# Performance work log

Hardware: AMD Instinct MI355X
Metric: run time of the kernel (lower is better)

Reference implementation:

```python
import jax, jax.numpy as jnp
import numpy as np

B, EMBED, HIDDEN, C, E = 1024, 768, 2048, 200, 256
LS = 0.1  # rbf_lengthscale
EPS = 1e-5


def setup_inputs() -> dict:
    key = jax.random.key(0)
    ks = jax.random.split(key, 10)
    inp = {
        'features': jax.random.normal(ks[0], (B, EMBED), jnp.float32),
        # MLP layer 1: LayerNorm(EMBED) -> Linear(EMBED, HIDDEN)
        'ln1_g': jnp.ones((EMBED,), jnp.float32),
        'ln1_b': jnp.zeros((EMBED,), jnp.float32),
        'W1': jax.random.normal(ks[1], (EMBED, HIDDEN), jnp.float32) / np.sqrt(EMBED),
        'b1': jnp.zeros((HIDDEN,), jnp.float32),
        # MLP layer 2: LayerNorm(HIDDEN) -> Linear(HIDDEN, HIDDEN)
        'ln2_g': jnp.ones((HIDDEN,), jnp.float32),
        'ln2_b': jnp.zeros((HIDDEN,), jnp.float32),
        'W2': jax.random.normal(ks[2], (HIDDEN, HIDDEN), jnp.float32) / np.sqrt(HIDDEN),
        'b2': jnp.zeros((HIDDEN,), jnp.float32),
        # final projection to centroid_dim
        'W3': jax.random.normal(ks[3], (HIDDEN, E), jnp.float32) / np.sqrt(HIDDEN),
        'b3': jnp.zeros((E,), jnp.float32),
        # per-class transform + centroids (as in torch init)
        'class_weight': jax.random.normal(ks[4], (C, E, E), jnp.float32) * 0.01,
        'centroids': jax.random.normal(ks[5], (C, E), jnp.float32) * 0.05,
    }
    return inp


def _layernorm(x, g, b):
    mu = jnp.mean(x, axis=-1, keepdims=True)
    var = jnp.var(x, axis=-1, keepdims=True)
    return (x - mu) * jax.lax.rsqrt(var + EPS) * g + b


def reference(features, ln1_g, ln1_b, W1, b1, ln2_g, ln2_b, W2, b2, W3, b3,
              class_weight, centroids):
    # feature_extractor MLP (dropout is identity at inference)
    h = _layernorm(features, ln1_g, ln1_b)
    h = jax.nn.gelu(h @ W1 + b1, approximate=False)
    h = _layernorm(h, ln2_g, ln2_b)
    h = jax.nn.gelu(h @ W2 + b2, approximate=False)
    z = h @ W3 + b3  # [B, E]

    # per-class transform: einsum('bce,ced->bcd') with z broadcast over C
    weighted = jnp.einsum('be,ced->bcd', z, class_weight)  # [B, C, E]
    diff = weighted - centroids[None, :, :]
    dist_sq = jnp.sum(diff * diff, axis=-1)  # [B, C]
    log_kernel = -dist_sq / (2.0 * LS * LS)
    kernel_vals = jnp.exp(log_kernel)
    probs = jax.nn.softmax(log_kernel, axis=-1)
    uncertainty = 1.0 - jnp.max(kernel_vals, axis=-1)
    return probs, probs[None], kernel_vals, uncertainty
```

## Files before the change

kernel.cpp:

```cpp
#include <hip/hip_runtime.h>
#include <math.h>

#define B_      1024
#define EMBED_  768
#define HIDDEN_ 2048
#define C_      200
#define E_      256
#define EPS_    1e-5f
#define NEG_INV_2LS2 (-50.0f)

typedef unsigned short ushort_t;
typedef __attribute__((ext_vector_type(8))) short short8;
typedef __attribute__((ext_vector_type(4))) float f32x4;

__device__ __forceinline__ float gelu_exact(float x) {
    return 0.5f * x * (1.0f + erff(x * 0.70710678118654752f));
}

__device__ __forceinline__ ushort_t f2bf(float x) {
    union { float f; unsigned int u; } v; v.f = x;
    unsigned int r = v.u + 0x7fffu + ((v.u >> 16) & 1u);
    return (ushort_t)(r >> 16);
}
__device__ __forceinline__ float bf2f(ushort_t s) {
    union { float f; unsigned int u; } v; v.u = ((unsigned int)s) << 16;
    return v.f;
}

__device__ __forceinline__ void glds16(const void* g, void* l) {
    __builtin_amdgcn_global_load_lds(
        (const __attribute__((address_space(1))) unsigned int*)g,
        (__attribute__((address_space(3))) unsigned int*)l, 16, 0, 0);
}

template<int COLS>
__global__ __launch_bounds__(256)
void ln_split_kernel(const float* __restrict__ x, const float* __restrict__ g,
                     const float* __restrict__ b, ushort_t* __restrict__ oh,
                     ushort_t* __restrict__ ol) {
    const int row = blockIdx.x;
    const int tid = threadIdx.x;
    constexpr int NT  = 256;
    constexpr int PER = COLS / NT;
    float v[PER];
    float s = 0.f, s2 = 0.f;
    const float* xr = x + (size_t)row * COLS;
    #pragma unroll
    for (int i = 0; i < PER; ++i) {
        v[i] = xr[tid + i * NT];
        s  += v[i];
        s2 += v[i] * v[i];
    }
    #pragma unroll
    for (int off = 32; off > 0; off >>= 1) {
        s  += __shfl_down(s,  off, 64);
        s2 += __shfl_down(s2, off, 64);
    }
    __shared__ float sbuf[4], s2buf[4], stat[2];
    const int wid = tid >> 6;
    if ((tid & 63) == 0) { sbuf[wid] = s; s2buf[wid] = s2; }
    __syncthreads();
    if (tid == 0) {
        float ts = 0.f, ts2 = 0.f;
        #pragma unroll
        for (int i = 0; i < NT / 64; ++i) { ts += sbuf[i]; ts2 += s2buf[i]; }
        float mu  = ts / COLS;
        float var = ts2 / COLS - mu * mu;
        stat[0] = mu;
        stat[1] = rsqrtf(var + EPS_);
    }
    __syncthreads();
    const float mu = stat[0], rstd = stat[1];
    #pragma unroll
    for (int i = 0; i < PER; ++i) {
        int c = tid + i * NT;
        float y = (v[i] - mu) * rstd * g[c] + b[c];
        ushort_t h = f2bf(y);
        size_t o = (size_t)row * COLS + c;
        oh[o] = h;
        ol[o] = f2bf(y - bf2f(h));
    }
}

__global__ __launch_bounds__(256)
void tconv_kernel(const float* __restrict__ src, ushort_t* __restrict__ th,
                  ushort_t* __restrict__ tl, int R, int Nc) {
    __shared__ float tile[64][65];
    const size_t base = (size_t)blockIdx.x * R * Nc;
    const int ntx = Nc >> 6;
    const int ky = blockIdx.y / ntx, nx = blockIdx.y % ntx;
    const int tid = threadIdx.x;
    const int col = tid & 63, rr = tid >> 6;
    const float* s = src + base + (size_t)(ky * 64) * Nc + nx * 64;
    #pragma unroll
    for (int i = 0; i < 16; ++i) {
        int r = i * 4 + rr;
        tile[r][col] = s[(size_t)r * Nc + col];
    }
    __syncthreads();
    #pragma unroll
    for (int i = 0; i < 16; ++i) {
        int dl = i * 4 + rr;
        float x = tile[col][dl];
        ushort_t h = f2bf(x);
        size_t o = base + (size_t)(nx * 64 + dl) * R + ky * 64 + col;
        th[o] = h;
        tl[o] = f2bf(x - bf2f(h));
    }
}

template<int MREP, int ACT, int OUT_SPLIT>
__global__ __launch_bounds__(256)
void mfma_gemm_kernel(const ushort_t* __restrict__ Ah, const ushort_t* __restrict__ Al,
                      const ushort_t* __restrict__ Wh, const ushort_t* __restrict__ Wl,
                      const float* __restrict__ bias,
                      float* __restrict__ outF, ushort_t* __restrict__ Oh,
                      ushort_t* __restrict__ Ol, int M, int N, int K) {
    constexpr int BM = MREP * 32;
    __shared__ short AsH[BM * 64], AsL[BM * 64];
    __shared__ short BsH[64 * 64], BsL[64 * 64];
    const int tid  = threadIdx.x;
    const int lane = tid & 63;
    const int w    = tid >> 6;
    const int wr = w >> 1, wc = w & 1;
    const int fr = lane & 15, fg = lane >> 4;

    const int nblk = gridDim.x, chunk = nblk >> 3;
    const int wg = (blockIdx.x & 7) * chunk + (blockIdx.x >> 3);
    const int gy = M / BM;
    const int cx = wg / gy, ry = wg % gy;
    const int row0 = ry * BM, col0 = cx * 64;

    const int srow  = tid >> 3;
    const int sslot = (tid & 7) ^ (srow & 7);
    const size_t aoff = (size_t)(row0 + srow) * K + sslot * 8;
    const size_t boff = (size_t)(col0 + srow) * K + sslot * 8;

    f32x4 acc[MREP][2];
    #pragma unroll
    for (int m = 0; m < MREP; ++m)
        #pragma unroll
        for (int n = 0; n < 2; ++n) acc[m][n] = (f32x4){0.f, 0.f, 0.f, 0.f};

    for (int k0 = 0; k0 < K; k0 += 64) {
        #pragma unroll
        for (int p = 0; p < BM / 32; ++p) {
            glds16(Ah + aoff + (size_t)p * 32 * K + k0, &AsH[p * 2048 + w * 512]);
            glds16(Al + aoff + (size_t)p * 32 * K + k0, &AsL[p * 2048 + w * 512]);
        }
        #pragma unroll
        for (int p = 0; p < 2; ++p) {
            glds16(Wh + boff + (size_t)p * 32 * K + k0, &BsH[p * 2048 + w * 512]);
            glds16(Wl + boff + (size_t)p * 32 * K + k0, &BsL[p * 2048 + w * 512]);
        }
        __syncthreads();
        #pragma unroll
        for (int ks = 0; ks < 2; ++ks) {
            short8 bh[2], bl[2];
            #pragma unroll
            for (int n = 0; n < 2; ++n) {
                int rB = wc * 32 + n * 16 + fr;
                int sl = ((ks * 4 + fg) ^ (rB & 7)) << 3;
                bh[n] = *(const short8*)&BsH[rB * 64 + sl];
                bl[n] = *(const short8*)&BsL[rB * 64 + sl];
            }
            #pragma unroll
            for (int m = 0; m < MREP; ++m) {
                int rA = wr * MREP * 16 + m * 16 + fr;
                int sl = ((ks * 4 + fg) ^ (rA & 7)) << 3;
                short8 ah = *(const short8*)&AsH[rA * 64 + sl];
                short8 al = *(const short8*)&AsL[rA * 64 + sl];
                #pragma unroll
                for (int n = 0; n < 2; ++n) {
                    acc[m][n] = __builtin_amdgcn_mfma_f32_16x16x32_bf16(ah, bh[n], acc[m][n], 0, 0, 0);
                    acc[m][n] = __builtin_amdgcn_mfma_f32_16x16x32_bf16(ah, bl[n], acc[m][n], 0, 0, 0);
                    acc[m][n] = __builtin_amdgcn_mfma_f32_16x16x32_bf16(al, bh[n], acc[m][n], 0, 0, 0);
                }
            }
        }
        __syncthreads();
    }

    #pragma unroll
    for (int n = 0; n < 2; ++n) {
        int col = col0 + wc * 32 + n * 16 + fr;
        float bv = bias[col];
        #pragma unroll
        for (int m = 0; m < MREP; ++m) {
            #pragma unroll
            for (int r = 0; r < 4; ++r) {
                int row = row0 + wr * MREP * 16 + m * 16 + fg * 4 + r;
                float v = acc[m][n][r] + bv;
                if (ACT) v = gelu_exact(v);
                size_t o = (size_t)row * N + col;
                if (OUT_SPLIT) {
                    ushort_t h = f2bf(v);
                    Oh[o] = h;
                    Ol[o] = f2bf(v - bf2f(h));
                } else {
                    outF[o] = v;
                }
            }
        }
    }
}

__global__ __launch_bounds__(256)
void rbf_mfma_kernel(const ushort_t* __restrict__ zh,
                     const ushort_t* __restrict__ zl,
                     const ushort_t* __restrict__ cwh,
                     const ushort_t* __restrict__ cwl,
                     const float* __restrict__ cent,
                     float* __restrict__ logk) {
    __shared__ short Ah[64 * 32], Al[64 * 32];
    __shared__ short Bh[256 * 32], Bl[256 * 32];
    __shared__ float red[64][4];

    const int tid  = threadIdx.x;
    const int lane = tid & 63;
    const int w    = tid >> 6;
    const int fr   = lane & 15;
    const int fg   = lane >> 4;

    const int bid = blockIdx.x;
    const int wg  = (bid & 7) * 400 + (bid >> 3);
    const int c    = wg >> 4;
    const int row0 = (wg & 15) * 64;

    const int srow = tid >> 2;
    const int sw   = ((tid & 3) ^ (srow & 3)) * 8;
    const ushort_t* gAh = zh + (size_t)(row0 + srow) * E_ + sw;
    const ushort_t* gAl = zl + (size_t)(row0 + srow) * E_ + sw;
    const ushort_t* gBh = cwh + (size_t)c * 65536 + (size_t)srow * E_ + sw;
    const ushort_t* gBl = cwl + (size_t)c * 65536 + (size_t)srow * E_ + sw;

    f32x4 acc[4][4];
    #pragma unroll
    for (int m = 0; m < 4; ++m)
        #pragma unroll
        for (int n = 0; n < 4; ++n)
            acc[m][n] = (f32x4){0.f, 0.f, 0.f, 0.f};

    for (int k0 = 0; k0 < 8; ++k0) {
        const int ke = k0 * 32;
        glds16(gAh + ke, &Ah[w * 512]);
        glds16(gAl + ke, &Al[w * 512]);
        #pragma unroll
        for (int i = 0; i < 4; ++i) {
            glds16(gBh + (size_t)i * 64 * E_ + ke, &Bh[i * 2048 + w * 512]);
            glds16(gBl + (size_t)i * 64 * E_ + ke, &Bl[i * 2048 + w * 512]);
        }
        __syncthreads();

        short8 bh[4], bl[4];
        #pragma unroll
        for (int n = 0; n < 4; ++n) {
            int d = w * 64 + n * 16 + fr;
            int sl = (fg ^ (d & 3)) << 3;
            bh[n] = *(const short8*)&Bh[d * 32 + sl];
            bl[n] = *(const short8*)&Bl[d * 32 + sl];
        }
        #pragma unroll
        for (int m = 0; m < 4; ++m) {
            int r = m * 16 + fr;
            int sa = (fg ^ (r & 3)) << 3;
            short8 ah = *(const short8*)&Ah[r * 32 + sa];
            short8 al = *(const short8*)&Al[r * 32 + sa];
            #pragma unroll
            for (int n = 0; n < 4; ++n) {
                acc[m][n] = __builtin_amdgcn_mfma_f32_16x16x32_bf16(ah, bh[n], acc[m][n], 0, 0, 0);
                acc[m][n] = __builtin_amdgcn_mfma_f32_16x16x32_bf16(ah, bl[n], acc[m][n], 0, 0, 0);
                acc[m][n] = __builtin_amdgcn_mfma_f32_16x16x32_bf16(al, bh[n], acc[m][n], 0, 0, 0);
            }
        }
        __syncthreads();
    }

    float cmu[4];
    #pragma unroll
    for (int n = 0; n < 4; ++n) cmu[n] = cent[(size_t)c * E_ + w * 64 + n * 16 + fr];

    #pragma unroll
    for (int m = 0; m < 4; ++m) {
        #pragma unroll
        for (int r = 0; r < 4; ++r) {
            float p = 0.f;
            #pragma unroll
            for (int n = 0; n < 4; ++n) {
                float d = acc[m][n][r] - cmu[n];
                p = fmaf(d, d, p);
            }
            p += __shfl_xor(p, 1, 64);
            p += __shfl_xor(p, 2, 64);
            p += __shfl_xor(p, 4, 64);
            p += __shfl_xor(p, 8, 64);
            if (fr == 0) red[m * 16 + fg * 4 + r][w] = p;
        }
    }
    __syncthreads();
    if (tid < 64) {
        float s = red[tid][0] + red[tid][1] + red[tid][2] + red[tid][3];
        logk[(size_t)(row0 + tid) * C_ + c] = NEG_INV_2LS2 * s;
    }
}

__global__ __launch_bounds__(64)
void out_kernel(const float* __restrict__ logk, float* __restrict__ dout) {
    const int b = blockIdx.x;
    const int t = threadIdx.x;
    const float* lr = logk + (size_t)b * C_;
    float v[4];
    float m = -INFINITY;
    #pragma unroll
    for (int i = 0; i < 4; ++i) {
        int idx = t + i * 64;
        v[i] = (idx < C_) ? lr[idx] : -INFINITY;
        m = fmaxf(m, v[i]);
    }
    #pragma unroll
    for (int off = 32; off > 0; off >>= 1) m = fmaxf(m, __shfl_xor(m, off, 64));
    float s = 0.f;
    #pragma unroll
    for (int i = 0; i < 4; ++i) {
        int idx = t + i * 64;
        if (idx < C_) s += expf(v[i] - m);
    }
    #pragma unroll
    for (int off = 32; off > 0; off >>= 1) s += __shfl_xor(s, off, 64);
    const float inv = 1.0f / s;
    #pragma unroll
    for (int i = 0; i < 4; ++i) {
        int idx = t + i * 64;
        if (idx < C_) {
            float p = expf(v[i] - m) * inv;
            dout[(size_t)b * C_ + idx] = p;
            dout[(size_t)204800 + (size_t)b * C_ + idx] = p;
            dout[(size_t)409600 + (size_t)b * C_ + idx] = expf(v[i]);
        }
    }
    if (t == 0) dout[(size_t)614400 + b] = 1.0f - expf(m);
}

extern "C" void kernel_launch(void* const* d_in, const int* in_sizes, int n_in,
                              void* d_out, int out_size, void* d_ws, size_t ws_size,
                              hipStream_t stream) {
    const float* features = (const float*)d_in[0];
    const float* ln1_g = (const float*)d_in[1];
    const float* ln1_b = (const float*)d_in[2];
    const float* W1    = (const float*)d_in[3];
    const float* b1    = (const float*)d_in[4];
    const float* ln2_g = (const float*)d_in[5];
    const float* ln2_b = (const float*)d_in[6];
    const float* W2    = (const float*)d_in[7];
    const float* b2    = (const float*)d_in[8];
    const float* W3    = (const float*)d_in[9];
    const float* b3    = (const float*)d_in[10];
    const float* cw    = (const float*)d_in[11];
    const float* cent  = (const float*)d_in[12];
    float* out = (float*)d_out;
    float* ws  = (float*)d_ws;

    float* h1 = ws;
    float* lk = ws + 2097152;
    ushort_t* u = (ushort_t*)(ws + 2097152 + 204800);
    size_t o = 0;
    ushort_t* h0h = u + o; o += (size_t)B_ * EMBED_;
    ushort_t* h0l = u + o; o += (size_t)B_ * EMBED_;
    ushort_t* h1h = u + o; o += (size_t)B_ * HIDDEN_;
    ushort_t* h1l = u + o; o += (size_t)B_ * HIDDEN_;
    ushort_t* h2h = u + o; o += (size_t)B_ * HIDDEN_;
    ushort_t* h2l = u + o; o += (size_t)B_ * HIDDEN_;
    ushort_t* zh  = u + o; o += (size_t)B_ * E_;
    ushort_t* zl  = u + o; o += (size_t)B_ * E_;
    ushort_t* w1h = u + o; o += (size_t)EMBED_ * HIDDEN_;
    ushort_t* w1l = u + o; o += (size_t)EMBED_ * HIDDEN_;
    ushort_t* w2h = u + o; o += (size_t)HIDDEN_ * HIDDEN_;
    ushort_t* w2l = u + o; o += (size_t)HIDDEN_ * HIDDEN_;
    ushort_t* w3h = u + o; o += (size_t)HIDDEN_ * E_;
    ushort_t* w3l = u + o; o += (size_t)HIDDEN_ * E_;
    ushort_t* cwh = u + o; o += (size_t)C_ * E_ * E_;
    ushort_t* cwl = u + o; o += (size_t)C_ * E_ * E_;

    tconv_kernel<<<dim3(C_, 16), 256, 0, stream>>>(cw, cwh, cwl, E_, E_);
    tconv_kernel<<<dim3(1, (EMBED_ / 64) * (HIDDEN_ / 64)), 256, 0, stream>>>(W1, w1h, w1l, EMBED_, HIDDEN_);
    tconv_kernel<<<dim3(1, (HIDDEN_ / 64) * (HIDDEN_ / 64)), 256, 0, stream>>>(W2, w2h, w2l, HIDDEN_, HIDDEN_);
    tconv_kernel<<<dim3(1, (HIDDEN_ / 64) * (E_ / 64)), 256, 0, stream>>>(W3, w3h, w3l, HIDDEN_, E_);

    ln_split_kernel<EMBED_><<<B_, 256, 0, stream>>>(features, ln1_g, ln1_b, h0h, h0l);

    mfma_gemm_kernel<2, 1, 0><<<(HIDDEN_ / 64) * (B_ / 64), 256, 0, stream>>>(
        h0h, h0l, w1h, w1l, b1, h1, nullptr, nullptr, B_, HIDDEN_, EMBED_);

    ln_split_kernel<HIDDEN_><<<B_, 256, 0, stream>>>(h1, ln2_g, ln2_b, h1h, h1l);

    mfma_gemm_kernel<2, 1, 1><<<(HIDDEN_ / 64) * (B_ / 64), 256, 0, stream>>>(
        h1h, h1l, w2h, w2l, b2, nullptr, h2h, h2l, B_, HIDDEN_, HIDDEN_);

    mfma_gemm_kernel<1, 0, 1><<<(E_ / 64) * (B_ / 32), 256, 0, stream>>>(
        h2h, h2l, w3h, w3l, b3, nullptr, zh, zl, B_, E_, HIDDEN_);

    rbf_mfma_kernel<<<3200, 256, 0, stream>>>(zh, zl, cwh, cwl, cent, lk);

    out_kernel<<<B_, 64, 0, stream>>>(lk, out);
}
```

Baseline: 341.5 us.

## Double-buffer RBF kernel LDS staging to overlap global loads with MFMA

Converts the RBF class-transform kernel to a two-stage software pipeline: it issues the next K-slice's direct-to-LDS loads before computing on the current buffer, waiting on a partial vmcnt. The hi and lo bf16 halves now share one interleaved 64-wide row with an 8-way XOR swizzle, and shared memory becomes dynamic (80 KB). The aim is to hide global load latency behind MFMA work. The cost is double the LDS footprint, which lowers the number of blocks resident per CU.

Result: faster. 320.5 us (-6.2%).

```diff
diff --git a/kernel.cpp b/kernel.cpp
--- a/kernel.cpp
+++ b/kernel.cpp
@@ -212,10 +212,7 @@
                      const ushort_t* __restrict__ cwl,
                      const float* __restrict__ cent,
                      float* __restrict__ logk) {
-    __shared__ short Ah[64 * 32], Al[64 * 32];
-    __shared__ short Bh[256 * 32], Bl[256 * 32];
-    __shared__ float red[64][4];
-
+    extern __shared__ short smem[];
     const int tid  = threadIdx.x;
     const int lane = tid & 63;
     const int w    = tid >> 6;
@@ -227,12 +224,13 @@
     const int c    = wg >> 4;
     const int row0 = (wg & 15) * 64;
 
-    const int srow = tid >> 2;
-    const int sw   = ((tid & 3) ^ (srow & 3)) * 8;
-    const ushort_t* gAh = zh + (size_t)(row0 + srow) * E_ + sw;
-    const ushort_t* gAl = zl + (size_t)(row0 + srow) * E_ + sw;
-    const ushort_t* gBh = cwh + (size_t)c * 65536 + (size_t)srow * E_ + sw;
-    const ushort_t* gBl = cwl + (size_t)c * 65536 + (size_t)srow * E_ + sw;
+    const int srow8 = tid >> 3;
+    const int ss    = (tid & 7) ^ (srow8 & 7);
+    const int kofs  = (ss & 3) * 8;
+    const ushort_t* zsel  = (ss < 4) ? zh  : zl;
+    const ushort_t* cwsel = (ss < 4) ? cwh : cwl;
+    const ushort_t* gA = zsel  + (size_t)(row0 + srow8) * E_ + kofs;
+    const ushort_t* gB = cwsel + (size_t)c * 65536 + (size_t)srow8 * E_ + kofs;
 
     f32x4 acc[4][4];
     #pragma unroll
@@ -241,31 +239,33 @@
         for (int n = 0; n < 4; ++n)
             acc[m][n] = (f32x4){0.f, 0.f, 0.f, 0.f};
 
-    for (int k0 = 0; k0 < 8; ++k0) {
-        const int ke = k0 * 32;
-        glds16(gAh + ke, &Ah[w * 512]);
-        glds16(gAl + ke, &Al[w * 512]);
-        #pragma unroll
-        for (int i = 0; i < 4; ++i) {
-            glds16(gBh + (size_t)i * 64 * E_ + ke, &Bh[i * 2048 + w * 512]);
-            glds16(gBl + (size_t)i * 64 * E_ + ke, &Bl[i * 2048 + w * 512]);
-        }
-        __syncthreads();
-
+    auto STAGE = [&](int t, int buf) {
+        const int ke = t * 32;
+        #pragma unroll
+        for (int i = 0; i < 2; ++i)
+            glds16(gA + (size_t)i * 32 * E_ + ke,
+                   &smem[buf * 4096 + i * 2048 + w * 512]);
+        #pragma unroll
+        for (int i = 0; i < 8; ++i)
+            glds16(gB + (size_t)i * 32 * E_ + ke,
+                   &smem[8192 + buf * 16384 + i * 2048 + w * 512]);
+    };
+
+    auto COMPUTE = [&](int buf) {
+        const short* Ab = &smem[buf * 4096];
+        const short* Bb = &smem[8192 + buf * 16384];
         short8 bh[4], bl[4];
         #pragma unroll
         for (int n = 0; n < 4; ++n) {
             int d = w * 64 + n * 16 + fr;
-            int sl = (fg ^ (d & 3)) << 3;
-            bh[n] = *(const short8*)&Bh[d * 32 + sl];
-            bl[n] = *(const short8*)&Bl[d * 32 + sl];
+            bh[n] = *(const short8*)&Bb[d * 64 + ((fg       ^ (d & 7)) << 3)];
+            bl[n] = *(const short8*)&Bb[d * 64 + (((4 + fg) ^ (d & 7)) << 3)];
         }
         #pragma unroll
         for (int m = 0; m < 4; ++m) {
             int r = m * 16 + fr;
-            int sa = (fg ^ (r & 3)) << 3;
-            short8 ah = *(const short8*)&Ah[r * 32 + sa];
-            short8 al = *(const short8*)&Al[r * 32 + sa];
+            short8 ah = *(const short8*)&Ab[r * 64 + ((fg       ^ (r & 7)) << 3)];
+            short8 al = *(const short8*)&Ab[r * 64 + (((4 + fg) ^ (r & 7)) << 3)];
             #pragma unroll
             for (int n = 0; n < 4; ++n) {
                 acc[m][n] = __builtin_amdgcn_mfma_f32_16x16x32_bf16(ah, bh[n], acc[m][n], 0, 0, 0);
@@ -273,13 +273,28 @@
                 acc[m][n] = __builtin_amdgcn_mfma_f32_16x16x32_bf16(al, bh[n], acc[m][n], 0, 0, 0);
             }
         }
-        __syncthreads();
-    }
+    };
+
+    STAGE(0, 0);
+    for (int t = 0; t < 7; ++t) {
+        STAGE(t + 1, (t + 1) & 1);
+        asm volatile("s_waitcnt vmcnt(10)" ::: "memory");
+        __builtin_amdgcn_s_barrier();
+        __builtin_amdgcn_sched_barrier(0);
+        COMPUTE(t & 1);
+        __builtin_amdgcn_s_barrier();
+    }
+    asm volatile("s_waitcnt vmcnt(0)" ::: "memory");
+    __builtin_amdgcn_s_barrier();
+    __builtin_amdgcn_sched_barrier(0);
+    COMPUTE(1);
 
     float cmu[4];
     #pragma unroll
     for (int n = 0; n < 4; ++n) cmu[n] = cent[(size_t)c * E_ + w * 64 + n * 16 + fr];
 
+    __syncthreads();
+    float* red = (float*)smem;
     #pragma unroll
     for (int m = 0; m < 4; ++m) {
         #pragma unroll
@@ -294,12 +309,12 @@
             p += __shfl_xor(p, 2, 64);
             p += __shfl_xor(p, 4, 64);
             p += __shfl_xor(p, 8, 64);
-            if (fr == 0) red[m * 16 + fg * 4 + r][w] = p;
+            if (fr == 0) red[(m * 16 + fg * 4 + r) * 4 + w] = p;
         }
     }
     __syncthreads();
     if (tid < 64) {
-        float s = red[tid][0] + red[tid][1] + red[tid][2] + red[tid][3];
+        float s = red[tid * 4 + 0] + red[tid * 4 + 1] + red[tid * 4 + 2] + red[tid * 4 + 3];
         logk[(size_t)(row0 + tid) * C_ + c] = NEG_INV_2LS2 * s;
     }
 }
@@ -399,7 +414,7 @@
     mfma_gemm_kernel<1, 0, 1><<<(E_ / 64) * (B_ / 32), 256, 0, stream>>>(
         h2h, h2l, w3h, w3l, b3, nullptr, zh, zl, B_, E_, HIDDEN_);
 
-    rbf_mfma_kernel<<<3200, 256, 0, stream>>>(zh, zl, cwh, cwl, cent, lk);
+    rbf_mfma_kernel<<<3200, 256, 81920, stream>>>(zh, zl, cwh, cwl, cent, lk);
 
     out_kernel<<<B_, 64, 0, stream>>>(lk, out);
 }
```
